# Kernel tuning notes

Measured on AMD Instinct MI355X. Metric: run time of the kernel, lower is better.

## Reference

```python
import jax, jax.numpy as jnp
import numpy as np

POLY_DEGREE = 3
LOW, MID, HIGH = 3, 6, 9
K = LOW + MID + HIGH  # 18 total harmonics
NUM_POINTS = 128 ** 3
BATCH = 4


def _band_sum(t, a, b, omega):
    """sum_k a_k*cos(w_k t) + b_k*sin(w_k t) without materializing [B,N,K].
    t: [B,N]; a,b: [N,k]; omega: [k]. Scans over the small harmonic axis."""
    def step(acc, xs):
        a_k, b_k, w = xs  # a_k,b_k: [N], w: scalar
        ph = w * t  # [B,N]
        return acc + a_k[None, :] * jnp.cos(ph) + b_k[None, :] * jnp.sin(ph), None
    acc0 = jnp.zeros_like(t)
    acc, _ = jax.lax.scan(step, acc0, (a.T, b.T, omega))
    return acc


def setup_inputs() -> dict:
    key = jax.random.key(0)
    k1, k2, k3, k4 = jax.random.split(key, 4)
    input_t = jax.random.uniform(k1, (BATCH,), dtype=jnp.float32)  # times in [0,1)
    poly_coeffs = jax.random.normal(k2, (NUM_POINTS, POLY_DEGREE + 1), dtype=jnp.float32) * 0.1
    fourier_a = jax.random.normal(k3, (NUM_POINTS, K), dtype=jnp.float32) * 0.1
    fourier_b = jax.random.normal(k4, (NUM_POINTS, K), dtype=jnp.float32) * 0.1
    return {
        "input_t": input_t,
        "poly_coeffs": poly_coeffs,
        "fourier_a": fourier_a,
        "fourier_b": fourier_b,
        "model_stage": 3,
    }


def reference(input_t, poly_coeffs, fourier_a, fourier_b, model_stage):
    B = input_t.shape[0]
    N = poly_coeffs.shape[0]
    t = jnp.broadcast_to(input_t[:, None], (B, N))  # [B, N]
    curr_stage = min(model_stage, 3) if model_stage >= 0 else 3
    omega = 2.0 * jnp.pi * jnp.arange(1, K + 1, dtype=jnp.float32)

    y_poly = jnp.zeros((B, N), dtype=jnp.float32)
    if POLY_DEGREE > 0 and curr_stage >= 0:
        for i in range(POLY_DEGREE + 1):
            y_poly = y_poly + poly_coeffs[:, i][None, :] * t ** i

    y_fourier = jnp.zeros((B, N), dtype=jnp.float32)
    bands = [(0, LOW, 1), (LOW, LOW + MID, 2), (LOW + MID, K, 3)]
    for s, e, req_stage in bands:
        if e > s and curr_stage >= req_stage:
            y_fourier = y_fourier + _band_sum(
                t, fourier_a[:, s:e], fourier_b[:, s:e], omega[s:e]
            )
    return y_poly, y_fourier
```

## Files before the change

### kernel.cpp

```cpp
#include <hip/hip_runtime.h>

#define KH 18
#define NPTS (128*128*128)
#define BB 4
#define BLK 256

__global__ __launch_bounds__(BLK, 8) void dddm_kernel(
    const float* __restrict__ input_t,
    const float* __restrict__ poly,
    const float* __restrict__ fa,
    const float* __restrict__ fb,
    const int*   __restrict__ stage_p,
    float* __restrict__ out)
{
    const int tid = threadIdx.x;
    const int n   = blockIdx.x * BLK + tid;

    float tb[BB], c1[BB], s1[BB], d[BB];
#pragma unroll
    for (int b = 0; b < BB; ++b) {
        const float t = input_t[b];
        tb[b] = t;
        float sn, cs;
        sincosf(6.283185307179586f * t, &sn, &cs);
        c1[b] = cs; s1[b] = sn; d[b] = 2.0f * cs;
    }

    const int ms = *stage_p;
    const int cs_ = (ms >= 0) ? (ms < 3 ? ms : 3) : 3;
    const int kmax = (cs_ >= 3) ? 18 : (cs_ == 2 ? 9 : (cs_ == 1 ? 3 : 0));

    const float4 c4 = reinterpret_cast<const float4*>(poly)[n];
    float yp[BB], yf[BB];
#pragma unroll
    for (int b = 0; b < BB; ++b) {
        const float t = tb[b];
        yp[b] = ((c4.w * t + c4.z) * t + c4.y) * t + c4.x;
        yf[b] = 0.0f;
    }

    const float2* ar = reinterpret_cast<const float2*>(fa + (size_t)n * KH);
    const float2* br = reinterpret_cast<const float2*>(fb + (size_t)n * KH);

    if (kmax == KH) {
        float cc[BB], ss[BB], cp[BB], sp[BB];
#pragma unroll
        for (int b = 0; b < BB; ++b) {
            cc[b] = c1[b]; ss[b] = s1[b];
            cp[b] = 1.0f;  sp[b] = 0.0f;
        }
#pragma unroll
        for (int j = 0; j < 9; ++j) {
            const float2 a2 = ar[j];
            const float2 b2 = br[j];
#pragma unroll
            for (int u = 0; u < 2; ++u) {
                const float ak = u ? a2.y : a2.x;
                const float bk = u ? b2.y : b2.x;
#pragma unroll
                for (int b = 0; b < BB; ++b) {
                    yf[b] += ak * cc[b];
                    yf[b] += bk * ss[b];
                    const float cn = __builtin_fmaf(d[b], cc[b], -cp[b]);
                    const float s2 = __builtin_fmaf(d[b], ss[b], -sp[b]);
                    cp[b] = cc[b]; sp[b] = ss[b];
                    cc[b] = cn;    ss[b] = s2;
                }
            }
        }
    } else if (kmax > 0) {
        const float* arow = fa + (size_t)n * KH;
        const float* brow = fb + (size_t)n * KH;
        float cc[BB], ss[BB], cp[BB], sp[BB];
#pragma unroll
        for (int b = 0; b < BB; ++b) {
            cc[b] = c1[b]; ss[b] = s1[b];
            cp[b] = 1.0f;  sp[b] = 0.0f;
        }
        for (int k = 0; k < kmax; ++k) {
            const float ak = arow[k];
            const float bk = brow[k];
#pragma unroll
            for (int b = 0; b < BB; ++b) {
                yf[b] += ak * cc[b];
                yf[b] += bk * ss[b];
                const float cn = __builtin_fmaf(d[b], cc[b], -cp[b]);
                const float s2 = __builtin_fmaf(d[b], ss[b], -sp[b]);
                cp[b] = cc[b]; sp[b] = ss[b];
                cc[b] = cn;    ss[b] = s2;
            }
        }
    }

#pragma unroll
    for (int b = 0; b < BB; ++b) {
        out[(size_t)b * NPTS + n]        = yp[b];
        out[(size_t)(BB + b) * NPTS + n] = yf[b];
    }
}

extern "C" void kernel_launch(void* const* d_in, const int* in_sizes, int n_in,
                              void* d_out, int out_size, void* d_ws, size_t ws_size,
                              hipStream_t stream) {
    const float* input_t = (const float*)d_in[0];
    const float* poly    = (const float*)d_in[1];
    const float* fa      = (const float*)d_in[2];
    const float* fb      = (const float*)d_in[3];
    const int*   stage   = (const int*)d_in[4];
    float* out = (float*)d_out;

    dddm_kernel<<<NPTS / BLK, BLK, 0, stream>>>(input_t, poly, fa, fb, stage, out);
}
```

Before: 374.3 us.

## Stage Fourier coefficient rows through shared memory with coalesced float4 loads

```diff
diff --git a/kernel.cpp b/kernel.cpp
--- a/kernel.cpp
+++ b/kernel.cpp
@@ -4,8 +4,9 @@
 #define NPTS (128*128*128)
 #define BB 4
 #define BLK 256
+#define TILE (BLK * KH)
 
-__global__ __launch_bounds__(BLK, 8) void dddm_kernel(
+__global__ __launch_bounds__(BLK, 6) void dddm_kernel(
     const float* __restrict__ input_t,
     const float* __restrict__ poly,
     const float* __restrict__ fa,
@@ -13,8 +14,11 @@
     const int*   __restrict__ stage_p,
     float* __restrict__ out)
 {
+    __shared__ float s[TILE];
+
     const int tid = threadIdx.x;
-    const int n   = blockIdx.x * BLK + tid;
+    const int n0  = blockIdx.x * BLK;
+    const int n   = n0 + tid;
 
     float tb[BB], c1[BB], s1[BB], d[BB];
 #pragma unroll
@@ -26,9 +30,29 @@
         c1[b] = cs; s1[b] = sn; d[b] = 2.0f * cs;
     }
 
+    const float4* fa4 = reinterpret_cast<const float4*>(fa + (size_t)n0 * KH);
+    const float4* fb4 = reinterpret_cast<const float4*>(fb + (size_t)n0 * KH);
+    float4* s4 = reinterpret_cast<float4*>(s);
+
+    float4 va[4], vb[4];
+    float4 va5 = make_float4(0.f, 0.f, 0.f, 0.f);
+    float4 vb5 = make_float4(0.f, 0.f, 0.f, 0.f);
+#pragma unroll
+    for (int j = 0; j < 4; ++j) va[j] = fa4[j * BLK + tid];
+    if (tid < 128) va5 = fa4[4 * BLK + tid];
+#pragma unroll
+    for (int j = 0; j < 4; ++j) vb[j] = fb4[j * BLK + tid];
+    if (tid < 128) vb5 = fb4[4 * BLK + tid];
+
+#pragma unroll
+    for (int j = 0; j < 4; ++j) s4[j * BLK + tid] = va[j];
+    if (tid < 128) s4[4 * BLK + tid] = va5;
+
     const int ms = *stage_p;
     const int cs_ = (ms >= 0) ? (ms < 3 ? ms : 3) : 3;
     const int kmax = (cs_ >= 3) ? 18 : (cs_ == 2 ? 9 : (cs_ == 1 ? 3 : 0));
+
+    __syncthreads();
 
     const float4 c4 = reinterpret_cast<const float4*>(poly)[n];
     float yp[BB], yf[BB];
@@ -39,55 +63,82 @@
         yf[b] = 0.0f;
     }
 
-    const float2* ar = reinterpret_cast<const float2*>(fa + (size_t)n * KH);
-    const float2* br = reinterpret_cast<const float2*>(fb + (size_t)n * KH);
-
-    if (kmax == KH) {
-        float cc[BB], ss[BB], cp[BB], sp[BB];
+    {
+        const float2* ar = reinterpret_cast<const float2*>(s + tid * KH);
+        if (kmax == KH) {
+            float cc[BB], cp[BB];
 #pragma unroll
-        for (int b = 0; b < BB; ++b) {
-            cc[b] = c1[b]; ss[b] = s1[b];
-            cp[b] = 1.0f;  sp[b] = 0.0f;
-        }
+            for (int b = 0; b < BB; ++b) { cc[b] = c1[b]; cp[b] = 1.0f; }
 #pragma unroll
-        for (int j = 0; j < 9; ++j) {
-            const float2 a2 = ar[j];
-            const float2 b2 = br[j];
+            for (int j = 0; j < 9; ++j) {
+                const float2 a2 = ar[j];
 #pragma unroll
-            for (int u = 0; u < 2; ++u) {
-                const float ak = u ? a2.y : a2.x;
-                const float bk = u ? b2.y : b2.x;
+                for (int u = 0; u < 2; ++u) {
+                    const float ak = u ? a2.y : a2.x;
+#pragma unroll
+                    for (int b = 0; b < BB; ++b) {
+                        yf[b] = __builtin_fmaf(ak, cc[b], yf[b]);
+                        const float cn = __builtin_fmaf(d[b], cc[b], -cp[b]);
+                        cp[b] = cc[b]; cc[b] = cn;
+                    }
+                }
+            }
+        } else if (kmax > 0) {
+            float cc[BB], cp[BB];
+#pragma unroll
+            for (int b = 0; b < BB; ++b) { cc[b] = c1[b]; cp[b] = 1.0f; }
+            for (int k = 0; k < kmax; ++k) {
+                const float ak = s[tid * KH + k];
 #pragma unroll
                 for (int b = 0; b < BB; ++b) {
-                    yf[b] += ak * cc[b];
-                    yf[b] += bk * ss[b];
+                    yf[b] = __builtin_fmaf(ak, cc[b], yf[b]);
                     const float cn = __builtin_fmaf(d[b], cc[b], -cp[b]);
-                    const float s2 = __builtin_fmaf(d[b], ss[b], -sp[b]);
-                    cp[b] = cc[b]; sp[b] = ss[b];
-                    cc[b] = cn;    ss[b] = s2;
+                    cp[b] = cc[b]; cc[b] = cn;
                 }
             }
         }
-    } else if (kmax > 0) {
-        const float* arow = fa + (size_t)n * KH;
-        const float* brow = fb + (size_t)n * KH;
-        float cc[BB], ss[BB], cp[BB], sp[BB];
+    }
+
+    __syncthreads();
+
 #pragma unroll
-        for (int b = 0; b < BB; ++b) {
-            cc[b] = c1[b]; ss[b] = s1[b];
-            cp[b] = 1.0f;  sp[b] = 0.0f;
-        }
-        for (int k = 0; k < kmax; ++k) {
-            const float ak = arow[k];
-            const float bk = brow[k];
+    for (int j = 0; j < 4; ++j) s4[j * BLK + tid] = vb[j];
+    if (tid < 128) s4[4 * BLK + tid] = vb5;
+
+    __syncthreads();
+
+    {
+        const float2* br = reinterpret_cast<const float2*>(s + tid * KH);
+        if (kmax == KH) {
+            float ss[BB], sp[BB];
 #pragma unroll
-            for (int b = 0; b < BB; ++b) {
-                yf[b] += ak * cc[b];
-                yf[b] += bk * ss[b];
-                const float cn = __builtin_fmaf(d[b], cc[b], -cp[b]);
-                const float s2 = __builtin_fmaf(d[b], ss[b], -sp[b]);
-                cp[b] = cc[b]; sp[b] = ss[b];
-                cc[b] = cn;    ss[b] = s2;
+            for (int b = 0; b < BB; ++b) { ss[b] = s1[b]; sp[b] = 0.0f; }
+#pragma unroll
+            for (int j = 0; j < 9; ++j) {
+                const float2 b2 = br[j];
+#pragma unroll
+                for (int u = 0; u < 2; ++u) {
+                    const float bk = u ? b2.y : b2.x;
+#pragma unroll
+                    for (int b = 0; b < BB; ++b) {
+                        yf[b] = __builtin_fmaf(bk, ss[b], yf[b]);
+                        const float sn = __builtin_fmaf(d[b], ss[b], -sp[b]);
+                        sp[b] = ss[b]; ss[b] = sn;
+                    }
+                }
+            }
+        } else if (kmax > 0) {
+            float ss[BB], sp[BB];
+#pragma unroll
+            for (int b = 0; b < BB; ++b) { ss[b] = s1[b]; sp[b] = 0.0f; }
+            for (int k = 0; k < kmax; ++k) {
+                const float bk = s[tid * KH + k];
+#pragma unroll
+                for (int b = 0; b < BB; ++b) {
+                    yf[b] = __builtin_fmaf(bk, ss[b], yf[b]);
+                    const float sn = __builtin_fmaf(d[b], ss[b], -sp[b]);
+                    sp[b] = ss[b]; ss[b] = sn;
+                }
             }
         }
     }
```

Result: no change. 376.6 us (+0.6%).

## Stage Fourier coefficient tiles through LDS with coalesced float4 loads

Applied to the files above, without the earlier changes.

```diff
diff --git a/kernel.cpp b/kernel.cpp
--- a/kernel.cpp
+++ b/kernel.cpp
@@ -4,8 +4,9 @@
 #define NPTS (128*128*128)
 #define BB 4
 #define BLK 256
+#define TILE (BLK * KH)
 
-__global__ __launch_bounds__(BLK, 8) void dddm_kernel(
+__global__ __launch_bounds__(BLK, 4) void dddm_kernel(
     const float* __restrict__ input_t,
     const float* __restrict__ poly,
     const float* __restrict__ fa,
@@ -13,42 +14,60 @@
     const int*   __restrict__ stage_p,
     float* __restrict__ out)
 {
+    __shared__ float s[2 * TILE];
+    __shared__ float seedT[BB], seedC[BB], seedS[BB];
+
     const int tid = threadIdx.x;
-    const int n   = blockIdx.x * BLK + tid;
+    const int n0  = blockIdx.x * BLK;
+    const int n   = n0 + tid;
 
-    float tb[BB], c1[BB], s1[BB], d[BB];
-#pragma unroll
-    for (int b = 0; b < BB; ++b) {
-        const float t = input_t[b];
-        tb[b] = t;
+    if (tid < BB) {
+        const float t = input_t[tid];
         float sn, cs;
         sincosf(6.283185307179586f * t, &sn, &cs);
-        c1[b] = cs; s1[b] = sn; d[b] = 2.0f * cs;
+        seedT[tid] = t; seedC[tid] = cs; seedS[tid] = sn;
+    }
+
+    const float4* fa4 = reinterpret_cast<const float4*>(fa + (size_t)n0 * KH);
+    const float4* fb4 = reinterpret_cast<const float4*>(fb + (size_t)n0 * KH);
+    float4* s4 = reinterpret_cast<float4*>(s);
+
+    float4 v[9];
+#pragma unroll
+    for (int j = 0; j < 9; ++j) {
+        const int idx = j * BLK + tid;
+        v[j] = (idx < TILE / 4) ? fa4[idx] : fb4[idx - TILE / 4];
+    }
+#pragma unroll
+    for (int j = 0; j < 9; ++j) {
+        const int idx = j * BLK + tid;
+        s4[idx] = v[j];
     }
 
     const int ms = *stage_p;
     const int cs_ = (ms >= 0) ? (ms < 3 ? ms : 3) : 3;
     const int kmax = (cs_ >= 3) ? 18 : (cs_ == 2 ? 9 : (cs_ == 1 ? 3 : 0));
 
+    __syncthreads();
+
     const float4 c4 = reinterpret_cast<const float4*>(poly)[n];
-    float yp[BB], yf[BB];
+    float d[BB], cc[BB], ss[BB], cp[BB], sp[BB], yp[BB], yf[BB];
 #pragma unroll
     for (int b = 0; b < BB; ++b) {
-        const float t = tb[b];
+        const float t  = seedT[b];
+        const float c1 = seedC[b];
+        const float s1 = seedS[b];
         yp[b] = ((c4.w * t + c4.z) * t + c4.y) * t + c4.x;
+        cc[b] = c1; ss[b] = s1;
+        cp[b] = 1.0f; sp[b] = 0.0f;
+        d[b]  = 2.0f * c1;
         yf[b] = 0.0f;
     }
 
-    const float2* ar = reinterpret_cast<const float2*>(fa + (size_t)n * KH);
-    const float2* br = reinterpret_cast<const float2*>(fb + (size_t)n * KH);
+    const float2* ar = reinterpret_cast<const float2*>(s + tid * KH);
+    const float2* br = reinterpret_cast<const float2*>(s + TILE + tid * KH);
 
     if (kmax == KH) {
-        float cc[BB], ss[BB], cp[BB], sp[BB];
-#pragma unroll
-        for (int b = 0; b < BB; ++b) {
-            cc[b] = c1[b]; ss[b] = s1[b];
-            cp[b] = 1.0f;  sp[b] = 0.0f;
-        }
 #pragma unroll
         for (int j = 0; j < 9; ++j) {
             const float2 a2 = ar[j];
@@ -59,35 +78,27 @@
                 const float bk = u ? b2.y : b2.x;
 #pragma unroll
                 for (int b = 0; b < BB; ++b) {
-                    yf[b] += ak * cc[b];
-                    yf[b] += bk * ss[b];
+                    yf[b] = __builtin_fmaf(ak, cc[b], yf[b]);
+                    yf[b] = __builtin_fmaf(bk, ss[b], yf[b]);
                     const float cn = __builtin_fmaf(d[b], cc[b], -cp[b]);
-                    const float s2 = __builtin_fmaf(d[b], ss[b], -sp[b]);
-                    cp[b] = cc[b]; sp[b] = ss[b];
-                    cc[b] = cn;    ss[b] = s2;
+                    const float sn = __builtin_fmaf(d[b], ss[b], -sp[b]);
+                    cp[b] = cc[b]; cc[b] = cn;
+                    sp[b] = ss[b]; ss[b] = sn;
                 }
             }
         }
     } else if (kmax > 0) {
-        const float* arow = fa + (size_t)n * KH;
-        const float* brow = fb + (size_t)n * KH;
-        float cc[BB], ss[BB], cp[BB], sp[BB];
-#pragma unroll
-        for (int b = 0; b < BB; ++b) {
-            cc[b] = c1[b]; ss[b] = s1[b];
-            cp[b] = 1.0f;  sp[b] = 0.0f;
-        }
         for (int k = 0; k < kmax; ++k) {
-            const float ak = arow[k];
-            const float bk = brow[k];
+            const float ak = s[tid * KH + k];
+            const float bk = s[TILE + tid * KH + k];
 #pragma unroll
             for (int b = 0; b < BB; ++b) {
-                yf[b] += ak * cc[b];
-                yf[b] += bk * ss[b];
+                yf[b] = __builtin_fmaf(ak, cc[b], yf[b]);
+                yf[b] = __builtin_fmaf(bk, ss[b], yf[b]);
                 const float cn = __builtin_fmaf(d[b], cc[b], -cp[b]);
-                const float s2 = __builtin_fmaf(d[b], ss[b], -sp[b]);
-                cp[b] = cc[b]; sp[b] = ss[b];
-                cc[b] = cn;    ss[b] = s2;
+                const float sn = __builtin_fmaf(d[b], ss[b], -sp[b]);
+                cp[b] = cc[b]; cc[b] = cn;
+                sp[b] = ss[b]; ss[b] = sn;
             }
         }
     }
```

Measured after the change: 349.2 us. 1.07x faster.
